# Optimization experiments

Measured on AMD Instinct MI355X. Metric: run time of the kernel, lower is better.

The kernel has to match this reference:

```python
import jax, jax.numpy as jnp
import numpy as np

EPS_D = 1e-05
EPS_LOG = 1e-05
H_BAND = 0.5


def setup_inputs() -> dict:
    key = jax.random.key(0)
    k1, k2 = jax.random.split(key)
    N, C, Hh, Ww = 4, 256, 64, 64
    y = jax.random.normal(k1, (N, C, Hh, Ww), dtype=jnp.float32)
    y_hat = jax.random.normal(k2, (N, C, Hh, Ww), dtype=jnp.float32)
    return {"y": y, "y_hat": y_hat}


def contextual_loss(x, y, h=H_BAND):
    # x, y: (N, C, H, W)
    N, C, Hh, Ww = x.shape
    # mean over W, H, N of y -> per-channel mu, broadcast as (1, C, 1, 1)
    y_mu = y.mean(axis=3).mean(axis=2).mean(axis=0).reshape(1, C, 1, 1)
    x_c = x - y_mu
    y_c = y - y_mu
    x_n = x_c / jnp.linalg.norm(x_c, ord=2, axis=1, keepdims=True)
    y_n = y_c / jnp.linalg.norm(y_c, ord=2, axis=1, keepdims=True)
    x_n = x_n.reshape(N, C, Hh * Ww)  # (N, C, P)
    y_n = y_n.reshape(N, C, Hh * Ww)
    # cosine similarity: (N, P, P)
    cosine_sim = jnp.einsum('ncp,ncq->npq', x_n, y_n)
    d = 1.0 - cosine_sim
    d_min = jnp.min(d, axis=2, keepdims=True)
    d_tilde = d / (d_min + EPS_D)
    w = jnp.exp((1.0 - d_tilde) / h)
    cx_ij = w / jnp.sum(w, axis=2, keepdims=True)
    cx = jnp.mean(jnp.max(cx_ij, axis=1), axis=1)  # (N,)
    return jnp.mean(-jnp.log(cx + EPS_LOG))


def reference(y, y_hat):
    return contextual_loss(y, y_hat)
```

## Files before the change

kernel.cpp:

```cpp
#include <hip/hip_runtime.h>
#include <hip/hip_bf16.h>
#include <math.h>


namespace {
constexpr int NB = 4;
constexpr int C  = 256;
constexpr int P  = 4096;
constexpr float EPSD = 1e-5f;
constexpr float EPSL = 1e-5f;
constexpr float HB   = 0.5f;

constexpr size_t OFF_MU    = 0;
constexpr size_t OFF_XNT   = 256;
constexpr size_t OFF_YNT   = OFF_XNT + (size_t)NB * P * C / 2;
constexpr size_t OFF_RMAXH = OFF_YNT + (size_t)NB * P * C / 2;
constexpr size_t OFF_SUMH  = OFF_RMAXH + (size_t)NB * 2 * P;
constexpr size_t OFF_CMAXH = OFF_SUMH + (size_t)NB * 2 * P;
constexpr size_t OFF_RMAX  = OFF_CMAXH + (size_t)NB * 2 * P;
constexpr size_t OFF_ALPHA = OFF_RMAX + (size_t)NB * P;
constexpr size_t OFF_LROW  = OFF_ALPHA + (size_t)NB * P;
}

typedef __attribute__((ext_vector_type(8))) __bf16 bf16x8;
typedef __attribute__((ext_vector_type(16))) float f32x16;
typedef unsigned short u16;

__device__ __forceinline__ bf16x8 ldfrag(const u16* p) {
  return *reinterpret_cast<const bf16x8*>(p);
}
__device__ __forceinline__ void gload_lds16(const u16* g, u16* l) {
  __builtin_amdgcn_global_load_lds(
      (const __attribute__((address_space(1))) void*)g,
      (__attribute__((address_space(3))) void*)l, 16, 0, 0);
}
__device__ __forceinline__ f32x16 zero16() {
  f32x16 z;
#pragma unroll
  for (int i = 0; i < 16; ++i) z[i] = 0.f;
  return z;
}

__device__ __forceinline__ void stage_tile(const u16* __restrict__ src, int row0,
                                           u16* lds, int t) {
#pragma unroll
  for (int i = 0; i < 8; ++i) {
    const int g  = i * 512 + t;
    const int r  = g >> 5;
    const int gs = (g & 31) ^ (r & 15);
    gload_lds16(src + (size_t)(row0 + r) * 256 + gs * 8, lds + (size_t)g * 8);
  }
}

__global__ void k_mu(const float* __restrict__ yh, float* __restrict__ ws) {
  const int c = blockIdx.x;
  const int t = threadIdx.x;
  float s = 0.f;
  for (int n = 0; n < NB; ++n) {
    const float* base = yh + ((size_t)(n * C + c)) * P;
    for (int p = t; p < P; p += 256) s += base[p];
  }
  __shared__ float red[256];
  red[t] = s;
  __syncthreads();
  for (int w = 128; w > 0; w >>= 1) {
    if (t < w) red[t] += red[t + w];
    __syncthreads();
  }
  if (t == 0) ws[OFF_MU + c] = red[0] * (1.0f / (NB * P));
}

__global__ __launch_bounds__(256) void k_norm(const float* __restrict__ x,
                                              const float* __restrict__ yh,
                                              float* __restrict__ ws) {
  const int b     = blockIdx.x;
  const int arr   = b & 1;
  const int strip = (b >> 1) & 63;
  const int n     = b >> 7;
  const int t     = threadIdx.x;
  const int w     = t >> 6;
  const int l     = t & 63;

  __shared__ float mu_s[C];
  __shared__ float tile[64][257];
  __shared__ float red[4][64];
  __shared__ float invs[64];

  mu_s[t] = ws[OFF_MU + t];
  __syncthreads();

  const float* src = arr ? yh : x;
  const size_t base = ((size_t)n * C) * P + (size_t)strip * 64 + l;
  float ssq = 0.f;
  for (int cc = 0; cc < C; cc += 4) {
    const int c = cc + w;
    const float v = src[base + (size_t)c * P] - mu_s[c];
    tile[l][c] = v;
    ssq += v * v;
  }
  red[w][l] = ssq;
  __syncthreads();
  if (t < 64) invs[t] = 1.0f / sqrtf(red[0][t] + red[1][t] + red[2][t] + red[3][t]);
  __syncthreads();

  uint* dst = reinterpret_cast<uint*>(ws + (arr ? OFF_YNT : OFF_XNT));
  const int c2 = t & 127;
  const size_t drow = ((size_t)n * P + (size_t)strip * 64) * (C / 2);
  for (int it = 0; it < 32; ++it) {
    const int pl = it * 2 + (t >> 7);
    const float s  = invs[pl];
    const float v0 = tile[pl][2 * c2] * s;
    const float v1 = tile[pl][2 * c2 + 1] * s;
    const unsigned short u0 = __builtin_bit_cast(unsigned short, __float2bfloat16(v0));
    const unsigned short u1 = __builtin_bit_cast(unsigned short, __float2bfloat16(v1));
    dst[drow + (size_t)pl * (C / 2) + c2] = ((uint)u1 << 16) | u0;
  }
}

template <int PASS>
__global__ __launch_bounds__(512, 2) void k_row(float* __restrict__ ws) {
  const int t = threadIdx.x;
  const int wave = t >> 6, l = t & 63, l31 = l & 31, lh = l >> 5, l15 = l31 & 15;
  const int rt = wave >> 1, ct = wave & 1;
  const int bid = blockIdx.x;
  const int qhalf = bid & 1, n = (bid >> 1) & 3, strip = bid >> 3;
  const int p0 = strip * 128;
  const int qbase = qhalf * 2048;

  const u16* xn = reinterpret_cast<const u16*>(ws + OFF_XNT) + (size_t)n * P * C;
  const u16* yn = reinterpret_cast<const u16*>(ws + OFF_YNT) + (size_t)n * P * C;

  __shared__ __align__(16) u16 Bl[2][128 * 256];
  __shared__ float red[8][32];

  const u16* Ap = xn + (size_t)(p0 + rt * 32 + l31) * 256;
  bf16x8 af[16];
#pragma unroll
  for (int ks = 0; ks < 16; ++ks) af[ks] = ldfrag(Ap + (ks * 2 + lh) * 8);

  float av[16], arm[16];
  if (PASS == 1) {
#pragma unroll
    for (int r = 0; r < 16; ++r) {
      const int row = (r & 3) + 8 * (r >> 2) + 4 * lh;
      const int p = p0 + rt * 32 + row;
      const float a_ = ws[OFF_ALPHA + (size_t)n * P + p];
      av[r]  = a_;
      arm[r] = a_ * ws[OFF_RMAX + (size_t)n * P + p];
    }
  }

  float run[16];
#pragma unroll
  for (int r = 0; r < 16; ++r) run[r] = (PASS == 0) ? -3.0e38f : 0.f;

  stage_tile(yn, qbase, Bl[0], t);
  __syncthreads();

  const int r0 = ct * 64 + l31;

  for (int step = 0; step < 16; ++step) {
    const int cur = step & 1;
    if (step + 1 < 16) stage_tile(yn, qbase + (step + 1) * 128, Bl[cur ^ 1], t);
    const u16* Brow = &Bl[cur][(size_t)r0 * 256];

    f32x16 a00 = zero16(), a01 = zero16(), a10 = zero16(), a11 = zero16();
#pragma unroll
    for (int ks = 0; ks < 16; ks += 2) {
      const int g0 = ((ks * 2 + lh) ^ l15) * 8;
      const int g1 = ((ks * 2 + 2 + lh) ^ l15) * 8;
      a00 = __builtin_amdgcn_mfma_f32_32x32x16_bf16(af[ks], ldfrag(Brow + g0), a00, 0, 0, 0);
      a10 = __builtin_amdgcn_mfma_f32_32x32x16_bf16(af[ks], ldfrag(Brow + 32 * 256 + g0), a10, 0, 0, 0);
      a01 = __builtin_amdgcn_mfma_f32_32x32x16_bf16(af[ks + 1], ldfrag(Brow + g1), a01, 0, 0, 0);
      a11 = __builtin_amdgcn_mfma_f32_32x32x16_bf16(af[ks + 1], ldfrag(Brow + 32 * 256 + g1), a11, 0, 0, 0);
    }
    const f32x16 s0 = a00 + a01;
    const f32x16 s1 = a10 + a11;

    if (PASS == 0) {
#pragma unroll
      for (int r = 0; r < 16; ++r) run[r] = fmaxf(run[r], fmaxf(s0[r], s1[r]));
    } else {
#pragma unroll
      for (int r = 0; r < 16; ++r)
        run[r] += __expf(fmaf(av[r], s0[r], -arm[r])) + __expf(fmaf(av[r], s1[r], -arm[r]));
    }
    __syncthreads();
  }

#pragma unroll
  for (int m = 1; m <= 16; m <<= 1) {
#pragma unroll
    for (int r = 0; r < 16; ++r) {
      const float o = __shfl_xor(run[r], m, 64);
      run[r] = (PASS == 0) ? fmaxf(run[r], o) : (run[r] + o);
    }
  }
  if (l31 == 0) {
#pragma unroll
    for (int r = 0; r < 16; ++r)
      red[wave][(r & 3) + 8 * (r >> 2) + 4 * lh] = run[r];
  }
  __syncthreads();
  if (t < 128) {
    const int rt2 = t >> 5, row = t & 31;
    const float v0 = red[rt2 * 2][row], v1 = red[rt2 * 2 + 1][row];
    const size_t o = (size_t)(n * 2 + qhalf) * P + p0 + rt2 * 32 + row;
    if (PASS == 0)
      ws[OFF_RMAXH + o] = fmaxf(v0, v1);
    else
      ws[OFF_SUMH + o] = v0 + v1;
  }
}

__global__ void k_alpha(float* __restrict__ ws) {
  const int i = blockIdx.x * 256 + threadIdx.x;
  const int n = i >> 12, p = i & (P - 1);
  const float rm = fmaxf(ws[OFF_RMAXH + (size_t)(n * 2) * P + p],
                         ws[OFF_RMAXH + (size_t)(n * 2 + 1) * P + p]);
  ws[OFF_RMAX + (size_t)n * P + p]  = rm;
  ws[OFF_ALPHA + (size_t)n * P + p] = 1.0f / (HB * (1.0f - rm + EPSD));
}

__global__ void k_L(float* __restrict__ ws) {
  const int i = blockIdx.x * 256 + threadIdx.x;
  const int n = i >> 12, p = i & (P - 1);
  const float s = ws[OFF_SUMH + (size_t)(n * 2) * P + p] +
                  ws[OFF_SUMH + (size_t)(n * 2 + 1) * P + p];
  const float a_ = ws[OFF_ALPHA + (size_t)n * P + p];
  const float rm = ws[OFF_RMAX + (size_t)n * P + p];
  ws[OFF_LROW + (size_t)n * P + p] = fmaf(a_, rm, logf(s));
}

__global__ __launch_bounds__(512, 2) void k_col(float* __restrict__ ws) {
  const int t = threadIdx.x;
  const int wave = t >> 6, l = t & 63, l31 = l & 31, lh = l >> 5, l15 = l31 & 15;
  const int rt = wave >> 1, ct = wave & 1;
  const int bid = blockIdx.x;
  const int phalf = bid & 1, n = (bid >> 1) & 3, qstrip = bid >> 3;
  const int q0 = qstrip * 128;
  const int pbase = phalf * 2048;

  const u16* xn = reinterpret_cast<const u16*>(ws + OFF_XNT) + (size_t)n * P * C;
  const u16* yn = reinterpret_cast<const u16*>(ws + OFF_YNT) + (size_t)n * P * C;
  const float* alp = ws + OFF_ALPHA + (size_t)n * P;
  const float* lrw = ws + OFF_LROW + (size_t)n * P;

  __shared__ __align__(16) u16 Bl[2][128 * 256];
  __shared__ float red[8][32];

  const u16* Ap = yn + (size_t)(q0 + rt * 32 + l31) * 256;
  bf16x8 af[16];
#pragma unroll
  for (int ks = 0; ks < 16; ++ks) af[ks] = ldfrag(Ap + (ks * 2 + lh) * 8);

  float run[16];
#pragma unroll
  for (int r = 0; r < 16; ++r) run[r] = -3.0e38f;

  stage_tile(xn, pbase, Bl[0], t);
  __syncthreads();

  const int r0 = ct * 64 + l31;

  for (int step = 0; step < 16; ++step) {
    const int cur = step & 1;
    if (step + 1 < 16) stage_tile(xn, pbase + (step + 1) * 128, Bl[cur ^ 1], t);
    const u16* Brow = &Bl[cur][(size_t)r0 * 256];

    const int pc0 = pbase + step * 128 + ct * 64 + l31;
    const float a0 = alp[pc0],      L0 = lrw[pc0];
    const float a1 = alp[pc0 + 32], L1 = lrw[pc0 + 32];

    f32x16 a00 = zero16(), a01 = zero16(), a10 = zero16(), a11 = zero16();
#pragma unroll
    for (int ks = 0; ks < 16; ks += 2) {
      const int g0 = ((ks * 2 + lh) ^ l15) * 8;
      const int g1 = ((ks * 2 + 2 + lh) ^ l15) * 8;
      a00 = __builtin_amdgcn_mfma_f32_32x32x16_bf16(af[ks], ldfrag(Brow + g0), a00, 0, 0, 0);
      a10 = __builtin_amdgcn_mfma_f32_32x32x16_bf16(af[ks], ldfrag(Brow + 32 * 256 + g0), a10, 0, 0, 0);
      a01 = __builtin_amdgcn_mfma_f32_32x32x16_bf16(af[ks + 1], ldfrag(Brow + g1), a01, 0, 0, 0);
      a11 = __builtin_amdgcn_mfma_f32_32x32x16_bf16(af[ks + 1], ldfrag(Brow + 32 * 256 + g1), a11, 0, 0, 0);
    }
    const f32x16 s0 = a00 + a01;
    const f32x16 s1 = a10 + a11;
#pragma unroll
    for (int r = 0; r < 16; ++r)
      run[r] = fmaxf(run[r], fmaxf(fmaf(a0, s0[r], -L0), fmaf(a1, s1[r], -L1)));
    __syncthreads();
  }

#pragma unroll
  for (int m = 1; m <= 16; m <<= 1) {
#pragma unroll
    for (int r = 0; r < 16; ++r) run[r] = fmaxf(run[r], __shfl_xor(run[r], m, 64));
  }
  if (l31 == 0) {
#pragma unroll
    for (int r = 0; r < 16; ++r)
      red[wave][(r & 3) + 8 * (r >> 2) + 4 * lh] = run[r];
  }
  __syncthreads();
  if (t < 128) {
    const int rt2 = t >> 5, row = t & 31;
    const float v = fmaxf(red[rt2 * 2][row], red[rt2 * 2 + 1][row]);
    ws[OFF_CMAXH + (size_t)(n * 2 + phalf) * P + q0 + rt2 * 32 + row] = v;
  }
}

__global__ void k_final(const float* __restrict__ ws, float* __restrict__ out) {
  const int t = threadIdx.x;
  __shared__ float red[256];
  __shared__ float lsum_s;
  if (t == 0) lsum_s = 0.f;
  for (int n = 0; n < NB; ++n) {
    float e = 0.f;
    for (int q = t; q < P; q += 256) {
      const float m = fmaxf(ws[OFF_CMAXH + (size_t)(n * 2) * P + q],
                            ws[OFF_CMAXH + (size_t)(n * 2 + 1) * P + q]);
      e += __expf(m);
    }
    __syncthreads();
    red[t] = e;
    __syncthreads();
    for (int w = 128; w > 0; w >>= 1) {
      if (t < w) red[t] += red[t + w];
      __syncthreads();
    }
    if (t == 0) lsum_s += -logf(red[0] * (1.0f / P) + EPSL);
  }
  __syncthreads();
  if (t == 0) out[0] = lsum_s * 0.25f;
}

extern "C" void kernel_launch(void* const* d_in, const int* in_sizes, int n_in,
                              void* d_out, int out_size, void* d_ws, size_t ws_size,
                              hipStream_t stream) {
  const float* x  = (const float*)d_in[0];
  const float* yh = (const float*)d_in[1];
  float* ws  = (float*)d_ws;
  float* out = (float*)d_out;

  k_mu<<<dim3(C), dim3(256), 0, stream>>>(yh, ws);
  k_norm<<<dim3(NB * 64 * 2), dim3(256), 0, stream>>>(x, yh, ws);
  k_row<0><<<dim3(256), dim3(512), 0, stream>>>(ws);
  k_alpha<<<dim3(NB * P / 256), dim3(256), 0, stream>>>(ws);
  k_row<1><<<dim3(256), dim3(512), 0, stream>>>(ws);
  k_L<<<dim3(NB * P / 256), dim3(256), 0, stream>>>(ws);
  k_col<<<dim3(256), dim3(512), 0, stream>>>(ws);
  k_final<<<dim3(1), dim3(256), 0, stream>>>(ws, out);
}
```

Measured before the change: 173.5 us.

## Split GEMM passes into quarters with smaller LDS tiles and explicit waitcnt pipelining

Measured after the change: 538.2 us. 210% more time.

```diff
diff --git a/kernel.cpp b/kernel.cpp
--- a/kernel.cpp
+++ b/kernel.cpp
@@ -15,9 +15,9 @@
 constexpr size_t OFF_XNT   = 256;
 constexpr size_t OFF_YNT   = OFF_XNT + (size_t)NB * P * C / 2;
 constexpr size_t OFF_RMAXH = OFF_YNT + (size_t)NB * P * C / 2;
-constexpr size_t OFF_SUMH  = OFF_RMAXH + (size_t)NB * 2 * P;
-constexpr size_t OFF_CMAXH = OFF_SUMH + (size_t)NB * 2 * P;
-constexpr size_t OFF_RMAX  = OFF_CMAXH + (size_t)NB * 2 * P;
+constexpr size_t OFF_SUMH  = OFF_RMAXH + (size_t)NB * 4 * P;
+constexpr size_t OFF_CMAXH = OFF_SUMH + (size_t)NB * 4 * P;
+constexpr size_t OFF_RMAX  = OFF_CMAXH + (size_t)NB * 4 * P;
 constexpr size_t OFF_ALPHA = OFF_RMAX + (size_t)NB * P;
 constexpr size_t OFF_LROW  = OFF_ALPHA + (size_t)NB * P;
 }
@@ -41,10 +41,10 @@
   return z;
 }
 
-__device__ __forceinline__ void stage_tile(const u16* __restrict__ src, int row0,
-                                           u16* lds, int t) {
-#pragma unroll
-  for (int i = 0; i < 8; ++i) {
+__device__ __forceinline__ void stage_tile64(const u16* __restrict__ src, int row0,
+                                             u16* lds, int t) {
+#pragma unroll
+  for (int i = 0; i < 4; ++i) {
     const int g  = i * 512 + t;
     const int r  = g >> 5;
     const int gs = (g & 31) ^ (r & 15);
@@ -118,19 +118,19 @@
 }
 
 template <int PASS>
-__global__ __launch_bounds__(512, 2) void k_row(float* __restrict__ ws) {
+__global__ __launch_bounds__(512, 4) void k_row(float* __restrict__ ws) {
   const int t = threadIdx.x;
   const int wave = t >> 6, l = t & 63, l31 = l & 31, lh = l >> 5, l15 = l31 & 15;
   const int rt = wave >> 1, ct = wave & 1;
   const int bid = blockIdx.x;
-  const int qhalf = bid & 1, n = (bid >> 1) & 3, strip = bid >> 3;
+  const int qpart = bid & 3, n = (bid >> 2) & 3, strip = bid >> 4;
   const int p0 = strip * 128;
-  const int qbase = qhalf * 2048;
+  const int qbase = qpart * 1024;
 
   const u16* xn = reinterpret_cast<const u16*>(ws + OFF_XNT) + (size_t)n * P * C;
   const u16* yn = reinterpret_cast<const u16*>(ws + OFF_YNT) + (size_t)n * P * C;
 
-  __shared__ __align__(16) u16 Bl[2][128 * 256];
+  __shared__ __align__(16) u16 Bl[2][64 * 256];
   __shared__ float red[8][32];
 
   const u16* Ap = xn + (size_t)(p0 + rt * 32 + l31) * 256;
@@ -154,38 +154,40 @@
 #pragma unroll
   for (int r = 0; r < 16; ++r) run[r] = (PASS == 0) ? -3.0e38f : 0.f;
 
-  stage_tile(yn, qbase, Bl[0], t);
-  __syncthreads();
-
-  const int r0 = ct * 64 + l31;
+  stage_tile64(yn, qbase, Bl[0], t);
 
   for (int step = 0; step < 16; ++step) {
-    const int cur = step & 1;
-    if (step + 1 < 16) stage_tile(yn, qbase + (step + 1) * 128, Bl[cur ^ 1], t);
-    const u16* Brow = &Bl[cur][(size_t)r0 * 256];
-
-    f32x16 a00 = zero16(), a01 = zero16(), a10 = zero16(), a11 = zero16();
+    if (step + 1 < 16) {
+      stage_tile64(yn, qbase + (step + 1) * 64, Bl[(step + 1) & 1], t);
+      asm volatile("s_waitcnt vmcnt(4)" ::: "memory");
+    } else {
+      asm volatile("s_waitcnt vmcnt(0)" ::: "memory");
+    }
+    __builtin_amdgcn_sched_barrier(0);
+    __builtin_amdgcn_s_barrier();
+
+    const u16* Brow = &Bl[step & 1][(size_t)(ct * 32 + l31) * 256];
+    f32x16 a0 = zero16(), a1 = zero16();
+    __builtin_amdgcn_s_setprio(1);
 #pragma unroll
     for (int ks = 0; ks < 16; ks += 2) {
-      const int g0 = ((ks * 2 + lh) ^ l15) * 8;
-      const int g1 = ((ks * 2 + 2 + lh) ^ l15) * 8;
-      a00 = __builtin_amdgcn_mfma_f32_32x32x16_bf16(af[ks], ldfrag(Brow + g0), a00, 0, 0, 0);
-      a10 = __builtin_amdgcn_mfma_f32_32x32x16_bf16(af[ks], ldfrag(Brow + 32 * 256 + g0), a10, 0, 0, 0);
-      a01 = __builtin_amdgcn_mfma_f32_32x32x16_bf16(af[ks + 1], ldfrag(Brow + g1), a01, 0, 0, 0);
-      a11 = __builtin_amdgcn_mfma_f32_32x32x16_bf16(af[ks + 1], ldfrag(Brow + 32 * 256 + g1), a11, 0, 0, 0);
-    }
-    const f32x16 s0 = a00 + a01;
-    const f32x16 s1 = a10 + a11;
+      a0 = __builtin_amdgcn_mfma_f32_32x32x16_bf16(
+          af[ks], ldfrag(Brow + ((ks * 2 + lh) ^ l15) * 8), a0, 0, 0, 0);
+      a1 = __builtin_amdgcn_mfma_f32_32x32x16_bf16(
+          af[ks + 1], ldfrag(Brow + ((ks * 2 + 2 + lh) ^ l15) * 8), a1, 0, 0, 0);
+    }
+    __builtin_amdgcn_s_setprio(0);
+    const f32x16 s0 = a0 + a1;
 
     if (PASS == 0) {
 #pragma unroll
-      for (int r = 0; r < 16; ++r) run[r] = fmaxf(run[r], fmaxf(s0[r], s1[r]));
+      for (int r = 0; r < 16; ++r) run[r] = fmaxf(run[r], s0[r]);
     } else {
 #pragma unroll
-      for (int r = 0; r < 16; ++r)
-        run[r] += __expf(fmaf(av[r], s0[r], -arm[r])) + __expf(fmaf(av[r], s1[r], -arm[r]));
-    }
-    __syncthreads();
+      for (int r = 0; r < 16; ++r) run[r] += __expf(fmaf(av[r], s0[r], -arm[r]));
+    }
+    __builtin_amdgcn_sched_barrier(0);
+    __builtin_amdgcn_s_barrier();
   }
 
 #pragma unroll
@@ -205,7 +207,7 @@
   if (t < 128) {
     const int rt2 = t >> 5, row = t & 31;
     const float v0 = red[rt2 * 2][row], v1 = red[rt2 * 2 + 1][row];
-    const size_t o = (size_t)(n * 2 + qhalf) * P + p0 + rt2 * 32 + row;
+    const size_t o = (size_t)(n * 4 + qpart) * P + p0 + rt2 * 32 + row;
     if (PASS == 0)
       ws[OFF_RMAXH + o] = fmaxf(v0, v1);
     else
@@ -216,8 +218,10 @@
 __global__ void k_alpha(float* __restrict__ ws) {
   const int i = blockIdx.x * 256 + threadIdx.x;
   const int n = i >> 12, p = i & (P - 1);
-  const float rm = fmaxf(ws[OFF_RMAXH + (size_t)(n * 2) * P + p],
-                         ws[OFF_RMAXH + (size_t)(n * 2 + 1) * P + p]);
+  float rm = ws[OFF_RMAXH + (size_t)(n * 4) * P + p];
+#pragma unroll
+  for (int j = 1; j < 4; ++j)
+    rm = fmaxf(rm, ws[OFF_RMAXH + (size_t)(n * 4 + j) * P + p]);
   ws[OFF_RMAX + (size_t)n * P + p]  = rm;
   ws[OFF_ALPHA + (size_t)n * P + p] = 1.0f / (HB * (1.0f - rm + EPSD));
 }
@@ -225,28 +229,30 @@
 __global__ void k_L(float* __restrict__ ws) {
   const int i = blockIdx.x * 256 + threadIdx.x;
   const int n = i >> 12, p = i & (P - 1);
-  const float s = ws[OFF_SUMH + (size_t)(n * 2) * P + p] +
-                  ws[OFF_SUMH + (size_t)(n * 2 + 1) * P + p];
+  float s = 0.f;
+#pragma unroll
+  for (int j = 0; j < 4; ++j)
+    s += ws[OFF_SUMH + (size_t)(n * 4 + j) * P + p];
   const float a_ = ws[OFF_ALPHA + (size_t)n * P + p];
   const float rm = ws[OFF_RMAX + (size_t)n * P + p];
   ws[OFF_LROW + (size_t)n * P + p] = fmaf(a_, rm, logf(s));
 }
 
-__global__ __launch_bounds__(512, 2) void k_col(float* __restrict__ ws) {
+__global__ __launch_bounds__(512, 4) void k_col(float* __restrict__ ws) {
   const int t = threadIdx.x;
   const int wave = t >> 6, l = t & 63, l31 = l & 31, lh = l >> 5, l15 = l31 & 15;
   const int rt = wave >> 1, ct = wave & 1;
   const int bid = blockIdx.x;
-  const int phalf = bid & 1, n = (bid >> 1) & 3, qstrip = bid >> 3;
+  const int ppart = bid & 3, n = (bid >> 2) & 3, qstrip = bid >> 4;
   const int q0 = qstrip * 128;
-  const int pbase = phalf * 2048;
+  const int pbase = ppart * 1024;
 
   const u16* xn = reinterpret_cast<const u16*>(ws + OFF_XNT) + (size_t)n * P * C;
   const u16* yn = reinterpret_cast<const u16*>(ws + OFF_YNT) + (size_t)n * P * C;
   const float* alp = ws + OFF_ALPHA + (size_t)n * P;
   const float* lrw = ws + OFF_LROW + (size_t)n * P;
 
-  __shared__ __align__(16) u16 Bl[2][128 * 256];
+  __shared__ __align__(16) u16 Bl[2][64 * 256];
   __shared__ float red[8][32];
 
   const u16* Ap = yn + (size_t)(q0 + rt * 32 + l31) * 256;
@@ -258,36 +264,39 @@
 #pragma unroll
   for (int r = 0; r < 16; ++r) run[r] = -3.0e38f;
 
-  stage_tile(xn, pbase, Bl[0], t);
-  __syncthreads();
-
-  const int r0 = ct * 64 + l31;
+  stage_tile64(xn, pbase, Bl[0], t);
 
   for (int step = 0; step < 16; ++step) {
-    const int cur = step & 1;
-    if (step + 1 < 16) stage_tile(xn, pbase + (step + 1) * 128, Bl[cur ^ 1], t);
-    const u16* Brow = &Bl[cur][(size_t)r0 * 256];
-
-    const int pc0 = pbase + step * 128 + ct * 64 + l31;
-    const float a0 = alp[pc0],      L0 = lrw[pc0];
-    const float a1 = alp[pc0 + 32], L1 = lrw[pc0 + 32];
-
-    f32x16 a00 = zero16(), a01 = zero16(), a10 = zero16(), a11 = zero16();
+    if (step + 1 < 16) {
+      stage_tile64(xn, pbase + (step + 1) * 64, Bl[(step + 1) & 1], t);
+      asm volatile("s_waitcnt vmcnt(4)" ::: "memory");
+    } else {
+      asm volatile("s_waitcnt vmcnt(0)" ::: "memory");
+    }
+    __builtin_amdgcn_sched_barrier(0);
+    __builtin_amdgcn_s_barrier();
+
+    const int pc = pbase + step * 64 + ct * 32 + l31;
+    const float a_ = alp[pc];
+    const float L_ = lrw[pc];
+
+    const u16* Brow = &Bl[step & 1][(size_t)(ct * 32 + l31) * 256];
+    f32x16 a0 = zero16(), a1 = zero16();
+    __builtin_amdgcn_s_setprio(1);
 #pragma unroll
     for (int ks = 0; ks < 16; ks += 2) {
-      const int g0 = ((ks * 2 + lh) ^ l15) * 8;
-      const int g1 = ((ks * 2 + 2 + lh) ^ l15) * 8;
-      a00 = __builtin_amdgcn_mfma_f32_32x32x16_bf16(af[ks], ldfrag(Brow + g0), a00, 0, 0, 0);
-      a10 = __builtin_amdgcn_mfma_f32_32x32x16_bf16(af[ks], ldfrag(Brow + 32 * 256 + g0), a10, 0, 0, 0);
-      a01 = __builtin_amdgcn_mfma_f32_32x32x16_bf16(af[ks + 1], ldfrag(Brow + g1), a01, 0, 0, 0);
-      a11 = __builtin_amdgcn_mfma_f32_32x32x16_bf16(af[ks + 1], ldfrag(Brow + 32 * 256 + g1), a11, 0, 0, 0);
-    }
-    const f32x16 s0 = a00 + a01;
-    const f32x16 s1 = a10 + a11;
-#pragma unroll
-    for (int r = 0; r < 16; ++r)
-      run[r] = fmaxf(run[r], fmaxf(fmaf(a0, s0[r], -L0), fmaf(a1, s1[r], -L1)));
-    __syncthreads();
+      a0 = __builtin_amdgcn_mfma_f32_32x32x16_bf16(
+          af[ks], ldfrag(Brow + ((ks * 2 + lh) ^ l15) * 8), a0, 0, 0, 0);
+      a1 = __builtin_amdgcn_mfma_f32_32x32x16_bf16(
+          af[ks + 1], ldfrag(Brow + ((ks * 2 + 2 + lh) ^ l15) * 8), a1, 0, 0, 0);
+    }
+    __builtin_amdgcn_s_setprio(0);
+    const f32x16 s0 = a0 + a1;
+#pragma unroll
+    for (int r = 0; r < 16; ++r) run[r] = fmaxf(run[r], fmaf(a_, s0[r], -L_));
+
+    __builtin_amdgcn_sched_barrier(0);
+    __builtin_amdgcn_s_barrier();
   }
 
 #pragma unroll
@@ -304,7 +313,7 @@
   if (t < 128) {
     const int rt2 = t >> 5, row = t & 31;
     const float v = fmaxf(red[rt2 * 2][row], red[rt2 * 2 + 1][row]);
-    ws[OFF_CMAXH + (size_t)(n * 2 + phalf) * P + q0 + rt2 * 32 + row] = v;
+    ws[OFF_CMAXH + (size_t)(n * 4 + ppart) * P + q0 + rt2 * 32 + row] = v;
   }
 }
 
@@ -316,8 +325,10 @@
   for (int n = 0; n < NB; ++n) {
     float e = 0.f;
     for (int q = t; q < P; q += 256) {
-      const float m = fmaxf(ws[OFF_CMAXH + (size_t)(n * 2) * P + q],
-                            ws[OFF_CMAXH + (size_t)(n * 2 + 1) * P + q]);
+      float m = ws[OFF_CMAXH + (size_t)(n * 4) * P + q];
+#pragma unroll
+      for (int j = 1; j < 4; ++j)
+        m = fmaxf(m, ws[OFF_CMAXH + (size_t)(n * 4 + j) * P + q]);
       e += __expf(m);
     }
     __syncthreads();
@@ -343,10 +354,10 @@
 
   k_mu<<<dim3(C), dim3(256), 0, stream>>>(yh, ws);
   k_norm<<<dim3(NB * 64 * 2), dim3(256), 0, stream>>>(x, yh, ws);
-  k_row<0><<<dim3(256), dim3(512), 0, stream>>>(ws);
+  k_row<0><<<dim3(512), dim3(512), 0, stream>>>(ws);
   k_alpha<<<dim3(NB * P / 256), dim3(256), 0, stream>>>(ws);
-  k_row<1><<<dim3(256), dim3(512), 0, stream>>>(ws);
+  k_row<1><<<dim3(512), dim3(512), 0, stream>>>(ws);
   k_L<<<dim3(NB * P / 256), dim3(256), 0, stream>>>(ws);
-  k_col<<<dim3(256), dim3(512), 0, stream>>>(ws);
+  k_col<<<dim3(512), dim3(512), 0, stream>>>(ws);
   k_final<<<dim3(1), dim3(256), 0, stream>>>(ws, out);
 }
```
